# Kernel tuning notes

Measured on AMD Instinct MI355X. Metric: run time of the kernel, lower is better.

The kernel has to match this reference:

```python
import jax, jax.numpy as jnp
import numpy as np


def setup_inputs() -> dict:
    key = jax.random.key(0)
    X = jax.random.normal(key, (8, 64, 64, 64), dtype=jnp.float32)
    return {"X": X}


def reference(X):
    N, C, h, w = X.shape
    x1 = X.reshape(N, C, h * w)            # [N, C, HW]
    x2 = jnp.transpose(x1, (0, 2, 1))      # [N, HW, C]
    scores = jnp.einsum('bnc,bcm->bnm', x2, x1)  # [N, HW, HW]
    c = jax.nn.softmax(scores, axis=2)
    out = jnp.einsum('bnm,bmc->bnc', c, x2)      # [N, HW, C]
    out = jnp.transpose(out, (0, 2, 1)).reshape(N, C, h, w)
    return out
```

## Files before the change

kernel.cpp:

```cpp
#include <hip/hip_runtime.h>
#include <math.h>
#include <type_traits>


#define SEQ 4096
#define DIM 64
#define LDB 72
#define LDO 68
#define QSCALE 1.2011224087864498f

typedef __attribute__((ext_vector_type(8))) short  short8;
typedef __attribute__((ext_vector_type(4))) float  f32x4;

__device__ __forceinline__ unsigned short f2bf(float f) {
    union { float f; unsigned int u; } x; x.f = f;
    unsigned int u = x.u + 0x7FFFu + ((x.u >> 16) & 1u);
    return (unsigned short)(u >> 16);
}
__device__ __forceinline__ float bf2f(unsigned short h) {
    union { unsigned int u; float f; } x; x.u = ((unsigned int)h) << 16; return x.f;
}
__device__ __forceinline__ float fast_exp2(float x) {
#if __has_builtin(__builtin_amdgcn_exp2f)
    return __builtin_amdgcn_exp2f(x);
#else
    float r;
    asm("v_exp_f32 %0, %1\n\ts_nop 0" : "=v"(r) : "v"(x));
    return r;
#endif
}
__device__ __forceinline__ float fast_rcp(float x) {
#if __has_builtin(__builtin_amdgcn_rcpf)
    return __builtin_amdgcn_rcpf(x);
#else
    return 1.f / x;
#endif
}

#define LDT 68
__global__ __launch_bounds__(256) void prepass3(const float* __restrict__ X,
                                                unsigned short* __restrict__ Xbf,
                                                unsigned short* __restrict__ XbfT,
                                                float* __restrict__ Norms,
                                                float* __restrict__ MaxPart) {
    __shared__ __align__(16) unsigned short sT[64 * LDT];
    __shared__ float sRed[4];
    const int b = blockIdx.y, m0 = blockIdx.x * 64;
    const float* Xb = X + (size_t)b * DIM * SEQ;
    unsigned short* Bb = Xbf  + (size_t)b * DIM * SEQ;
    unsigned short* Tb = XbfT + (size_t)b * SEQ * DIM;
    const int t = threadIdx.x, w = t >> 6;
    const int mw = t & 15, cg = t >> 4;

    #pragma unroll
    for (int cr = 0; cr < 4; ++cr) {
        const int c = cg * 4 + cr;
        const f32x4 v = *(const f32x4*)(Xb + (size_t)c * SEQ + m0 + 4 * mw);
        *(ushort4*)(Bb + (size_t)c * SEQ + m0 + 4 * mw) =
            make_ushort4(f2bf(v.x), f2bf(v.y), f2bf(v.z), f2bf(v.w));
        sT[(4 * mw + 0) * LDT + c] = f2bf(v.x * QSCALE);
        sT[(4 * mw + 1) * LDT + c] = f2bf(v.y * QSCALE);
        sT[(4 * mw + 2) * LDT + c] = f2bf(v.z * QSCALE);
        sT[(4 * mw + 3) * LDT + c] = f2bf(v.w * QSCALE);
    }
    __syncthreads();
    const int m = t >> 2, ck = t & 3;
    const short8 a0 = *(const short8*)(sT + m * LDT + ck * 16);
    const short8 a1 = *(const short8*)(sT + m * LDT + ck * 16 + 8);
    *(short8*)(Tb + (size_t)(m0 + m) * DIM + ck * 16)     = a0;
    *(short8*)(Tb + (size_t)(m0 + m) * DIM + ck * 16 + 8) = a1;
    float s = 0.f;
    #pragma unroll
    for (int i = 0; i < 8; ++i) {
        const float f0 = bf2f((unsigned short)a0[i]);
        const float f1 = bf2f((unsigned short)a1[i]);
        s += f0 * f0 + f1 * f1;
    }
    s += __shfl_xor(s, 1);
    s += __shfl_xor(s, 2);
    const float nm = sqrtf(s);
    if (ck == 0) Norms[(size_t)b * SEQ + m0 + m] = nm;
    float mx = nm;
    #pragma unroll
    for (int d = 4; d < 64; d <<= 1) mx = fmaxf(mx, __shfl_xor(mx, d));
    if ((t & 63) == 0) sRed[w] = mx;
    __syncthreads();
    if (t == 0)
        MaxPart[b * 64 + blockIdx.x] =
            fmaxf(fmaxf(sRed[0], sRed[1]), fmaxf(sRed[2], sRed[3]));
}

template <bool PARTIAL>
__global__ __launch_bounds__(128, 4) void attn_split4(const unsigned short* __restrict__ Xbf,
                                                      const unsigned short* __restrict__ XbfT,
                                                      const float* __restrict__ Norms,
                                                      const float* __restrict__ MaxPart,
                                                      unsigned short* __restrict__ Obf,
                                                      float* __restrict__ Lbase,
                                                      float* __restrict__ Out,
                                                      int niter) {
    __shared__ __align__(16) unsigned char smem[20480];
    unsigned short* sK = (unsigned short*)smem;
    unsigned short* sV = (unsigned short*)(smem + 8192);
    unsigned short* sP = (unsigned short*)(smem + 16384);
    float*          sO = (float*)smem;

    const int tid  = threadIdx.x;
    const int lane = tid & 63;
    const int w    = tid >> 6;
    const int l15  = lane & 15;
    const int quad = lane >> 4;

    const int b   = blockIdx.y;
    const int s0  = blockIdx.x * 64;
    const int h   = blockIdx.z;
    const int kt0 = h * niter;
    const unsigned short* Bb = Xbf  + (size_t)b * DIM * SEQ;
    const unsigned short* Tb = XbfT + (size_t)b * SEQ * DIM;

    float mxn = MaxPart[b * 64 + lane];
    #pragma unroll
    for (int d = 1; d < 64; d <<= 1) mxn = fmaxf(mxn, __shfl_xor(mxn, d));

    short8 qf[2][2];
    f32x4 cin[2];
    #pragma unroll
    for (int qt = 0; qt < 2; ++qt) {
        const int row = s0 + 32 * w + 16 * qt + l15;
        const unsigned short* qp = Tb + (size_t)row * DIM + quad * 8;
        qf[qt][0] = *(const short8*)(qp);
        qf[qt][1] = *(const short8*)(qp + 32);
        const float mrow = Norms[(size_t)b * SEQ + row] * mxn;
        cin[qt] = (f32x4){-mrow, -mrow, -mrow, -mrow};
    }

    f32x4 acc_o[2][4];
    #pragma unroll
    for (int qt = 0; qt < 2; ++qt)
        #pragma unroll
        for (int ct = 0; ct < 4; ++ct) acc_o[qt][ct] = (f32x4){0.f, 0.f, 0.f, 0.f};
    f32x4 lp4[2];
    lp4[0] = (f32x4){0.f, 0.f, 0.f, 0.f};
    lp4[1] = (f32x4){0.f, 0.f, 0.f, 0.f};

    const int rsw  = l15 & 7;
    const int vkey = (l15 & 3) ^ (l15 >> 2);
    const unsigned short* kb[2];
    #pragma unroll
    for (int ks = 0; ks < 2; ++ks)
        kb[ks] = sK + (l15 << 6) + (((quad + 4 * ks) ^ rsw) << 3);
    const unsigned short* vb = sV + (l15 << 5) + ((quad ^ vkey) << 3);
    unsigned short* const prow = sP + (w << 10) + (l15 << 5);
    unsigned short* pw[2];
    #pragma unroll
    for (int mt = 0; mt < 2; ++mt)
        pw[mt] = prow + ((((2 * mt + (quad >> 1)) ^ vkey) << 3) + ((quad & 1) << 2));
    const unsigned short* pr = prow + ((quad ^ vkey) << 3);

    const int rl8 = lane >> 3, c8 = lane & 7;
    const int cgsK = c8 ^ rl8;
    const int rv = lane >> 2, cv = lane & 3;
    const int cvs = cv ^ ((rv & 3) ^ ((rv >> 2) & 3));
    const unsigned short* gK[2];
    const unsigned short* gV[2];
    #pragma unroll
    for (int j = 0; j < 2; ++j) {
        const int rowK = w * 16 + j * 8 + rl8;
        const int rowV = w * 32 + j * 16 + rv;
        gK[j] = Tb + (size_t)(kt0 * 32 + rowK) * 64 + cgsK * 8;
        gV[j] = Bb + (size_t)rowV * 4096 + kt0 * 32 + cvs * 8;
    }
    auto stageTo = [&](auto HC) {
        constexpr int HALF = decltype(HC)::value;
        #pragma unroll
        for (int j = 0; j < 2; ++j) {
            __builtin_amdgcn_global_load_lds(
                (const __attribute__((address_space(1))) unsigned int*)gK[j],
                (__attribute__((address_space(3))) unsigned int*)(sK + HALF * 2048 + (w * 16 + j * 8) * 64),
                16, 0, 0);
            __builtin_amdgcn_global_load_lds(
                (const __attribute__((address_space(1))) unsigned int*)gV[j],
                (__attribute__((address_space(3))) unsigned int*)(sV + HALF * 2048 + (w * 32 + j * 16) * 32),
                16, 0, 0);
        }
        #pragma unroll
        for (int j = 0; j < 2; ++j) { gK[j] += 2048; gV[j] += 32; }
    };

    auto computeT = [&](auto HC) {
        constexpr int HALF = decltype(HC)::value;
        short8 kf[2][2], vf[4];
        #pragma unroll
        for (int mt = 0; mt < 2; ++mt)
            #pragma unroll
            for (int ks = 0; ks < 2; ++ks)
                kf[ks][mt] = *(const short8*)(kb[ks] + HALF * 2048 + mt * 1024);
        #pragma unroll
        for (int ct = 0; ct < 4; ++ct)
            vf[ct] = *(const short8*)(vb + HALF * 2048 + ct * 512);

        f32x4 a[2][2];
        #pragma unroll
        for (int qt = 0; qt < 2; ++qt)
            #pragma unroll
            for (int mt = 0; mt < 2; ++mt) {
                f32x4 s = cin[qt];
                s = __builtin_amdgcn_mfma_f32_16x16x32_bf16(kf[0][mt], qf[qt][0], s, 0, 0, 0);
                s = __builtin_amdgcn_mfma_f32_16x16x32_bf16(kf[1][mt], qf[qt][1], s, 0, 0, 0);
                a[qt][mt] = s;
            }
        #pragma unroll
        for (int qt = 0; qt < 2; ++qt)
            #pragma unroll
            for (int mt = 0; mt < 2; ++mt) {
                const float p0 = fast_exp2(a[qt][mt][0]);
                const float p1 = fast_exp2(a[qt][mt][1]);
                const float p2 = fast_exp2(a[qt][mt][2]);
                const float p3 = fast_exp2(a[qt][mt][3]);
                lp4[qt] += (f32x4){p0, p1, p2, p3};
                const unsigned lo = __builtin_amdgcn_perm(__float_as_uint(p1), __float_as_uint(p0), 0x07060302u);
                const unsigned hi = __builtin_amdgcn_perm(__float_as_uint(p3), __float_as_uint(p2), 0x07060302u);
                *(uint2*)(pw[mt] + qt * 512) = make_uint2(lo, hi);
            }
        short8 pf[2];
        #pragma unroll
        for (int qt = 0; qt < 2; ++qt)
            pf[qt] = *(const short8*)(pr + qt * 512);
        #pragma unroll
        for (int qt = 0; qt < 2; ++qt)
            #pragma unroll
            for (int ct = 0; ct < 4; ++ct)
                acc_o[qt][ct] = __builtin_amdgcn_mfma_f32_16x16x32_bf16(pf[qt], vf[ct], acc_o[qt][ct], 0, 0, 0);
    };

    std::integral_constant<int, 0> H0;
    std::integral_constant<int, 1> H1;

    stageTo(H0);
    __syncthreads();
    for (int it = 0; it < niter; it += 2) {
        if (it + 1 < niter) stageTo(H1);
        computeT(H0);
        __syncthreads();
        if (it + 2 < niter) stageTo(H0);
        computeT(H1);
        __syncthreads();
    }

    float lp[2];
    #pragma unroll
    for (int qt = 0; qt < 2; ++qt) {
        lp[qt] = (lp4[qt][0] + lp4[qt][1]) + (lp4[qt][2] + lp4[qt][3]);
        lp[qt] += __shfl_xor(lp[qt], 16);
        lp[qt] += __shfl_xor(lp[qt], 32);
    }

    if (PARTIAL) {
        if (quad == 0) {
            #pragma unroll
            for (int qt = 0; qt < 2; ++qt)
                (Lbase + (size_t)h * 8 * SEQ)[(size_t)b * SEQ + s0 + 32 * w + 16 * qt + l15] = lp[qt];
        }
    } else {
        #pragma unroll
        for (int qt = 0; qt < 2; ++qt) {
            float inv[4];
            #pragma unroll
            for (int r = 0; r < 4; ++r) inv[r] = fast_rcp(__shfl(lp[qt], 4 * quad + r));
            #pragma unroll
            for (int ct = 0; ct < 4; ++ct)
                #pragma unroll
                for (int r = 0; r < 4; ++r) acc_o[qt][ct][r] *= inv[r];
        }
    }

    #pragma unroll
    for (int qt = 0; qt < 2; ++qt)
        #pragma unroll
        for (int ct = 0; ct < 4; ++ct) {
            const int c = 16 * ct + l15;
            #pragma unroll
            for (int r = 0; r < 4; ++r)
                sO[c * LDO + 32 * w + 16 * qt + 4 * quad + r] = acc_o[qt][ct][r];
        }
    __syncthreads();
    const int mw = tid & 15, cg = tid >> 4;
    if (PARTIAL) {
        unsigned short* Op = Obf + (size_t)h * 8 * DIM * SEQ;
        #pragma unroll
        for (int cc = 0; cc < 8; ++cc) {
            const int c = cg + 8 * cc;
            const f32x4 v = *(const f32x4*)(sO + c * LDO + 4 * mw);
            *(ushort4*)(Op + ((size_t)b * DIM + c) * SEQ + s0 + 4 * mw) =
                make_ushort4(f2bf(v.x), f2bf(v.y), f2bf(v.z), f2bf(v.w));
        }
    } else {
        #pragma unroll
        for (int cc = 0; cc < 8; ++cc) {
            const int c = cg + 8 * cc;
            const f32x4 v = *(const f32x4*)(sO + c * LDO + 4 * mw);
            *(f32x4*)(Out + ((size_t)b * DIM + c) * SEQ + s0 + 4 * mw) = v;
        }
    }
}

__global__ __launch_bounds__(256) void combine4(const unsigned short* __restrict__ Obf,
                                                const float* __restrict__ Lp,
                                                float* __restrict__ Out) {
    const int gid = blockIdx.x * 256 + threadIdx.x;
    const size_t base = (size_t)gid * 4;
    const int s = (int)(base & 4095);
    const int b = (int)(base >> 18);
    f32x4 os = (f32x4){0.f, 0.f, 0.f, 0.f};
    f32x4 ls = (f32x4){0.f, 0.f, 0.f, 0.f};
    #pragma unroll
    for (int h = 0; h < 4; ++h) {
        const ushort4 o = *(const ushort4*)(Obf + (size_t)h * 2097152 + base);
        os[0] += bf2f(o.x); os[1] += bf2f(o.y); os[2] += bf2f(o.z); os[3] += bf2f(o.w);
        const f32x4 l = *(const f32x4*)(Lp + (size_t)h * 8 * SEQ + b * SEQ + s);
        #pragma unroll
        for (int i = 0; i < 4; ++i) ls[i] += l[i];
    }
    f32x4 o;
    #pragma unroll
    for (int i = 0; i < 4; ++i) o[i] = os[i] / ls[i];
    *(f32x4*)(Out + base) = o;
}

__global__ __launch_bounds__(256, 2) void attn_fallback(const float* __restrict__ X,
                                                        float* __restrict__ Out) {
    __shared__ __align__(16) unsigned char smem[27648];
    unsigned short* sK = (unsigned short*)smem;
    unsigned short* sV = (unsigned short*)(smem + 9216);
    unsigned short* sP = (unsigned short*)(smem + 18432);
    float*          sO = (float*)smem;
    const int tid  = threadIdx.x;
    const int lane = tid & 63;
    const int w    = tid >> 6;
    const int l15  = lane & 15;
    const int quad = lane >> 4;
    const int b  = blockIdx.y;
    const int s0 = blockIdx.x * 64;
    const float* Xb = X + (size_t)b * DIM * SEQ;
    const int mgrp = tid & 15;
    const int c0   = tid >> 4;

    for (int cc = 0; cc < 4; ++cc) {
        int c = c0 + 16 * cc;
        const f32x4 v = *(const f32x4*)(Xb + (size_t)c * SEQ + s0 + 4 * mgrp);
        sK[(4 * mgrp + 0) * LDB + c] = f2bf(v.x);
        sK[(4 * mgrp + 1) * LDB + c] = f2bf(v.y);
        sK[(4 * mgrp + 2) * LDB + c] = f2bf(v.z);
        sK[(4 * mgrp + 3) * LDB + c] = f2bf(v.w);
    }
    __syncthreads();
    short8 qf0, qf1;
    {
        const int row = 16 * w + l15;
        qf0 = *(const short8*)(sK + row * LDB + quad * 8);
        qf1 = *(const short8*)(sK + row * LDB + 32 + quad * 8);
    }
    __syncthreads();
    f32x4 acc_o[4];
    for (int ct = 0; ct < 4; ++ct) acc_o[ct] = (f32x4){0.f, 0.f, 0.f, 0.f};
    float m_i[4] = {-1e30f, -1e30f, -1e30f, -1e30f};
    float l_i[4] = {0.f, 0.f, 0.f, 0.f};
    for (int kt = 0; kt < SEQ / 64; ++kt) {
        const int m0 = kt * 64;
        for (int cc = 0; cc < 4; ++cc) {
            int c = c0 + 16 * cc;
            const f32x4 v = *(const f32x4*)(Xb + (size_t)c * SEQ + m0 + 4 * mgrp);
            unsigned short h0 = f2bf(v.x), h1 = f2bf(v.y), h2 = f2bf(v.z), h3 = f2bf(v.w);
            *(ushort4*)(sV + c * LDB + 4 * mgrp) = make_ushort4(h0, h1, h2, h3);
            sK[(4 * mgrp + 0) * LDB + c] = h0;
            sK[(4 * mgrp + 1) * LDB + c] = h1;
            sK[(4 * mgrp + 2) * LDB + c] = h2;
            sK[(4 * mgrp + 3) * LDB + c] = h3;
        }
        __syncthreads();
        short8 vf[2][4];
        for (int ks = 0; ks < 2; ++ks)
            for (int ct = 0; ct < 4; ++ct)
                vf[ks][ct] = *(const short8*)(sV + (16 * ct + l15) * LDB + ks * 32 + quad * 8);
        f32x4 acc_s[4];
        for (int mt = 0; mt < 4; ++mt) {
            const int row = 16 * mt + l15;
            const short8 kf0 = *(const short8*)(sK + row * LDB + quad * 8);
            const short8 kf1 = *(const short8*)(sK + row * LDB + 32 + quad * 8);
            f32x4 a = (f32x4){0.f, 0.f, 0.f, 0.f};
            a = __builtin_amdgcn_mfma_f32_16x16x32_bf16(qf0, kf0, a, 0, 0, 0);
            a = __builtin_amdgcn_mfma_f32_16x16x32_bf16(qf1, kf1, a, 0, 0, 0);
            acc_s[mt] = a;
        }
        float alpha[4];
        for (int r = 0; r < 4; ++r) {
            float mx = fmaxf(fmaxf(acc_s[0][r], acc_s[1][r]), fmaxf(acc_s[2][r], acc_s[3][r]));
            mx = fmaxf(mx, __shfl_xor(mx, 1));
            mx = fmaxf(mx, __shfl_xor(mx, 2));
            mx = fmaxf(mx, __shfl_xor(mx, 4));
            mx = fmaxf(mx, __shfl_xor(mx, 8));
            const float mnew = fmaxf(m_i[r], mx);
            alpha[r] = __expf(m_i[r] - mnew);
            m_i[r] = mnew;
        }
        float rowsum[4] = {0.f, 0.f, 0.f, 0.f};
        unsigned short pb[4][4];
        for (int mt = 0; mt < 4; ++mt)
            for (int r = 0; r < 4; ++r) {
                const float p = __expf(acc_s[mt][r] - m_i[r]);
                rowsum[r] += p;
                pb[mt][r] = f2bf(p);
            }
        for (int r = 0; r < 4; ++r) {
            float s = rowsum[r];
            s += __shfl_xor(s, 1);
            s += __shfl_xor(s, 2);
            s += __shfl_xor(s, 4);
            s += __shfl_xor(s, 8);
            l_i[r] = alpha[r] * l_i[r] + s;
        }
        for (int ct = 0; ct < 4; ++ct)
            for (int r = 0; r < 4; ++r)
                acc_o[ct][r] *= alpha[r];
        for (int mt = 0; mt < 4; ++mt)
            for (int r = 0; r < 4; ++r)
                sP[(16 * w + quad * 4 + r) * LDB + l15 + 16 * mt] = pb[mt][r];
        __syncthreads();
        const short8 pf0 = *(const short8*)(sP + (16 * w + l15) * LDB + quad * 8);
        const short8 pf1 = *(const short8*)(sP + (16 * w + l15) * LDB + 32 + quad * 8);
        for (int ct = 0; ct < 4; ++ct) {
            acc_o[ct] = __builtin_amdgcn_mfma_f32_16x16x32_bf16(pf0, vf[0][ct], acc_o[ct], 0, 0, 0);
            acc_o[ct] = __builtin_amdgcn_mfma_f32_16x16x32_bf16(pf1, vf[1][ct], acc_o[ct], 0, 0, 0);
        }
    }
    float inv[4];
    for (int r = 0; r < 4; ++r) inv[r] = 1.f / l_i[r];
    for (int ct = 0; ct < 4; ++ct) {
        const int c = 16 * ct + l15;
        for (int r = 0; r < 4; ++r)
            sO[c * LDO + 16 * w + quad * 4 + r] = acc_o[ct][r] * inv[r];
    }
    __syncthreads();
    for (int cc = 0; cc < 4; ++cc) {
        const int c = c0 + 16 * cc;
        const f32x4 v = *(const f32x4*)(sO + c * LDO + 4 * mgrp);
        *(f32x4*)(Out + (size_t)b * DIM * SEQ + (size_t)c * SEQ + s0 + 4 * mgrp) = v;
    }
}

extern "C" void kernel_launch(void* const* d_in, const int* in_sizes, int n_in,
                              void* d_out, int out_size, void* d_ws, size_t ws_size,
                              hipStream_t stream) {
    const float* X = (const float*)d_in[0];
    float* Out = (float*)d_out;
    const size_t elems = (size_t)8 * SEQ * DIM;
    const size_t offXbfT  = elems * 2;
    const size_t offNorms = offXbfT + elems * 2;
    const size_t offMaxP  = offNorms + (size_t)8 * SEQ * 4;
    const size_t offObf   = offMaxP + 8 * 64 * 4;
    const size_t offLpart = offObf + 4 * elems * 2;
    const size_t need_split = offLpart + 4 * (size_t)8 * SEQ * 4;
    const size_t need_h1    = offObf;

    if (ws_size >= need_h1) {
        unsigned short* Xbf   = (unsigned short*)d_ws;
        unsigned short* XbfT  = (unsigned short*)((char*)d_ws + offXbfT);
        float* Norms   = (float*)((char*)d_ws + offNorms);
        float* MaxPart = (float*)((char*)d_ws + offMaxP);
        prepass3<<<dim3(64, 8), 256, 0, stream>>>(X, Xbf, XbfT, Norms, MaxPart);
        if (ws_size >= need_split) {
            unsigned short* Obf = (unsigned short*)((char*)d_ws + offObf);
            float* Lp = (float*)((char*)d_ws + offLpart);
            attn_split4<true><<<dim3(64, 8, 4), 128, 0, stream>>>(Xbf, XbfT, Norms, MaxPart,
                                                                  Obf, Lp, nullptr, 32);
            combine4<<<(int)(elems / 1024), 256, 0, stream>>>(Obf, Lp, Out);
        } else {
            attn_split4<false><<<dim3(64, 8, 1), 128, 0, stream>>>(Xbf, XbfT, Norms, MaxPart,
                                                                   nullptr, nullptr, Out, 128);
        }
    } else {
        attn_fallback<<<dim3(64, 8), 256, 0, stream>>>(X, Out);
    }
}
```

Baseline: 115.5 us.

## Load K/V fragments directly from global memory instead of LDS double-buffering

Removes the async global-to-LDS staging of K and V tiles, along with the double buffer and per-iteration block barriers. Each wave now reads its MFMA fragments straight from global memory (relying on L1/L2 caches), and LDS shrinks to the P scratch and output area. This cuts barrier and LDS traffic but exposes global-load latency with no prefetch. The two waves of a block also load the same K/V data redundantly.

```diff
diff --git a/kernel.cpp b/kernel.cpp
--- a/kernel.cpp
+++ b/kernel.cpp
@@ -1,6 +1,5 @@
 #include <hip/hip_runtime.h>
 #include <math.h>
-#include <type_traits>
 
 
 #define SEQ 4096
@@ -99,10 +98,8 @@
                                                       float* __restrict__ Lbase,
                                                       float* __restrict__ Out,
                                                       int niter) {
-    __shared__ __align__(16) unsigned char smem[20480];
-    unsigned short* sK = (unsigned short*)smem;
-    unsigned short* sV = (unsigned short*)(smem + 8192);
-    unsigned short* sP = (unsigned short*)(smem + 16384);
+    __shared__ __align__(16) unsigned char smem[17408];
+    unsigned short* sP = (unsigned short*)smem;
     float*          sO = (float*)smem;
 
     const int tid  = threadIdx.x;
@@ -143,13 +140,7 @@
     lp4[0] = (f32x4){0.f, 0.f, 0.f, 0.f};
     lp4[1] = (f32x4){0.f, 0.f, 0.f, 0.f};
 
-    const int rsw  = l15 & 7;
     const int vkey = (l15 & 3) ^ (l15 >> 2);
-    const unsigned short* kb[2];
-    #pragma unroll
-    for (int ks = 0; ks < 2; ++ks)
-        kb[ks] = sK + (l15 << 6) + (((quad + 4 * ks) ^ rsw) << 3);
-    const unsigned short* vb = sV + (l15 << 5) + ((quad ^ vkey) << 3);
     unsigned short* const prow = sP + (w << 10) + (l15 << 5);
     unsigned short* pw[2];
     #pragma unroll
@@ -157,47 +148,22 @@
         pw[mt] = prow + ((((2 * mt + (quad >> 1)) ^ vkey) << 3) + ((quad & 1) << 2));
     const unsigned short* pr = prow + ((quad ^ vkey) << 3);
 
-    const int rl8 = lane >> 3, c8 = lane & 7;
-    const int cgsK = c8 ^ rl8;
-    const int rv = lane >> 2, cv = lane & 3;
-    const int cvs = cv ^ ((rv & 3) ^ ((rv >> 2) & 3));
-    const unsigned short* gK[2];
-    const unsigned short* gV[2];
-    #pragma unroll
-    for (int j = 0; j < 2; ++j) {
-        const int rowK = w * 16 + j * 8 + rl8;
-        const int rowV = w * 32 + j * 16 + rv;
-        gK[j] = Tb + (size_t)(kt0 * 32 + rowK) * 64 + cgsK * 8;
-        gV[j] = Bb + (size_t)rowV * 4096 + kt0 * 32 + cvs * 8;
-    }
-    auto stageTo = [&](auto HC) {
-        constexpr int HALF = decltype(HC)::value;
-        #pragma unroll
-        for (int j = 0; j < 2; ++j) {
-            __builtin_amdgcn_global_load_lds(
-                (const __attribute__((address_space(1))) unsigned int*)gK[j],
-                (__attribute__((address_space(3))) unsigned int*)(sK + HALF * 2048 + (w * 16 + j * 8) * 64),
-                16, 0, 0);
-            __builtin_amdgcn_global_load_lds(
-                (const __attribute__((address_space(1))) unsigned int*)gV[j],
-                (__attribute__((address_space(3))) unsigned int*)(sV + HALF * 2048 + (w * 32 + j * 16) * 32),
-                16, 0, 0);
-        }
-        #pragma unroll
-        for (int j = 0; j < 2; ++j) { gK[j] += 2048; gV[j] += 32; }
-    };
-
-    auto computeT = [&](auto HC) {
-        constexpr int HALF = decltype(HC)::value;
+    const unsigned short* kp = Tb + (size_t)(kt0 * 32 + l15) * DIM + quad * 8;
+    const unsigned short* vp[4];
+    #pragma unroll
+    for (int ct = 0; ct < 4; ++ct)
+        vp[ct] = Bb + (size_t)(16 * ct + l15) * SEQ + kt0 * 32 + quad * 8;
+
+    for (int it = 0; it < niter; ++it) {
         short8 kf[2][2], vf[4];
         #pragma unroll
         for (int mt = 0; mt < 2; ++mt)
             #pragma unroll
             for (int ks = 0; ks < 2; ++ks)
-                kf[ks][mt] = *(const short8*)(kb[ks] + HALF * 2048 + mt * 1024);
+                kf[ks][mt] = *(const short8*)(kp + mt * 1024 + ks * 32);
         #pragma unroll
         for (int ct = 0; ct < 4; ++ct)
-            vf[ct] = *(const short8*)(vb + HALF * 2048 + ct * 512);
+            vf[ct] = *(const short8*)(vp[ct]);
 
         f32x4 a[2][2];
         #pragma unroll
@@ -231,20 +197,10 @@
             #pragma unroll
             for (int ct = 0; ct < 4; ++ct)
                 acc_o[qt][ct] = __builtin_amdgcn_mfma_f32_16x16x32_bf16(pf[qt], vf[ct], acc_o[qt][ct], 0, 0, 0);
-    };
-
-    std::integral_constant<int, 0> H0;
-    std::integral_constant<int, 1> H1;
-
-    stageTo(H0);
-    __syncthreads();
-    for (int it = 0; it < niter; it += 2) {
-        if (it + 1 < niter) stageTo(H1);
-        computeT(H0);
-        __syncthreads();
-        if (it + 2 < niter) stageTo(H0);
-        computeT(H1);
-        __syncthreads();
+
+        kp += 2048;
+        #pragma unroll
+        for (int ct = 0; ct < 4; ++ct) vp[ct] += 32;
     }
 
     float lp[2];
@@ -274,6 +230,7 @@
         }
     }
 
+    __syncthreads();
     #pragma unroll
     for (int qt = 0; qt < 2; ++qt)
         #pragma unroll
```

Result: slower. 188.4 us (+63.1%).
